# Optimization experiments

Hardware: AMD Instinct MI355X
Metric: run time of the kernel (lower is better)

The kernel has to match this reference:

```python
import jax, jax.numpy as jnp
import numpy as np

B, T, EMB, HS = 4, 4096, 1024, 64
BASE = 10000.0


def rope_angles(T, hs, base=BASE):
    # theta_i = base^(-2i/hs), freqs[t, i] = t * theta_i  -> (T, hs//2)
    inv = 1.0 / (base ** (2.0 * jnp.arange(hs // 2, dtype=jnp.float32) / hs))
    return jnp.arange(T, dtype=jnp.float32)[:, None] * inv[None, :]


def apply_rope(x, cos, sin):
    # x: (B, T, D); pairs are interleaved (even, odd) like torch.view_as_complex
    xr = x.reshape(*x.shape[:-1], -1, 2)
    xe, xo = xr[..., 0], xr[..., 1]
    re = xe * cos - xo * sin
    im = xe * sin + xo * cos
    return jnp.stack([re, im], axis=-1).reshape(x.shape)


def setup_inputs() -> dict:
    key = jax.random.key(0)
    kx, kq, kk, kv = jax.random.split(key, 4)
    s = 1.0 / np.sqrt(EMB)
    return {
        "x": jax.random.normal(kx, (B, T, EMB), jnp.float32),
        "Wq": jax.random.normal(kq, (HS, EMB), jnp.float32) * s,
        "Wk": jax.random.normal(kk, (HS, EMB), jnp.float32) * s,
        "Wv": jax.random.normal(kv, (HS, EMB), jnp.float32) * s,
    }


def reference(x, Wq, Wk, Wv):
    Tlen = x.shape[1]
    ang = rope_angles(Tlen, HS)          # (T, HS//2)
    cos, sin = jnp.cos(ang), jnp.sin(ang)
    q = x @ Wq.T                          # (B, T, HS)
    k = x @ Wk.T
    v = x @ Wv.T
    q = apply_rope(q, cos, sin)
    k = apply_rope(k, cos, sin)
    scores = jnp.einsum("bqd,bkd->bqk", q, k) * (HS ** -0.5)
    causal = jnp.tril(jnp.ones((Tlen, Tlen), dtype=bool))
    scores = jnp.where(causal[None], scores, -jnp.inf)
    w = jax.nn.softmax(scores, axis=-1)   # dropout in eval mode: identity
    return jnp.einsum("bqk,bkd->bqd", w, v)
```

## Files before the change

### kernel.cpp

```cpp
#include <hip/hip_runtime.h>

typedef __bf16 bf16x8 __attribute__((ext_vector_type(8)));
typedef __bf16 bf16x4 __attribute__((ext_vector_type(4)));
typedef float f32x4 __attribute__((ext_vector_type(4)));
typedef float f32x16 __attribute__((ext_vector_type(16)));
typedef unsigned int u32;

#define T_LEN 4096

__device__ __forceinline__ f32x4 mfma16(bf16x8 a, bf16x8 b, f32x4 c) {
    return __builtin_amdgcn_mfma_f32_16x16x32_bf16(a, b, c, 0, 0, 0);
}
__device__ __forceinline__ f32x16 mfma32(bf16x8 a, bf16x8 b, f32x16 c) {
    return __builtin_amdgcn_mfma_f32_32x32x16_bf16(a, b, c, 0, 0, 0);
}
__device__ __forceinline__ u32 packbf(float lo, float hi) {
    union { __bf16 e[2]; u32 w; } u;
    u.e[0] = (__bf16)lo; u.e[1] = (__bf16)hi;
    return u.w;
}
__device__ __forceinline__ f32x16 zero16() {
    f32x16 z;
    #pragma unroll
    for (int i = 0; i < 16; i++) z[i] = 0.f;
    return z;
}

__global__ __launch_bounds__(256) void convert_w_kernel(
    const float* __restrict__ Wq, const float* __restrict__ Wk,
    const float* __restrict__ Wv, __bf16* __restrict__ wb)
{
    int i = blockIdx.x * 256 + threadIdx.x;
    int m = i >> 14, off = (i & 16383) << 2;
    const float* s = (m == 0 ? Wq : (m == 1 ? Wk : Wv)) + off;
    float4 f = *(const float4*)s;
    bf16x4 h = { (__bf16)f.x, (__bf16)f.y, (__bf16)f.z, (__bf16)f.w };
    *(bf16x4*)(wb + (m << 16) + off) = h;
}

__global__ __launch_bounds__(512, 2) void proj_kernel(
    const float* __restrict__ x, const __bf16* __restrict__ wb,
    __bf16* __restrict__ qfb, __bf16* __restrict__ kfb, __bf16* __restrict__ vfb)
{
    __shared__ __bf16 smem[4608 + 27648];
    __bf16 (*xs)[32][72]  = (__bf16(*)[32][72])smem;
    __bf16 (*wl)[192][72] = (__bf16(*)[192][72])(smem + 4608);
    __bf16* stage = smem;

    const int tid  = threadIdx.x;
    const int wave = tid >> 6, lane = tid & 63;
    const int l15 = lane & 15, l4 = lane >> 4;
    const int wm = wave >> 2, wn = wave & 3;
    const size_t m0 = (size_t)blockIdx.x * 32;
    const int xrow = tid >> 4, xc4 = (tid & 15) * 4;
    const int wrow = tid >> 3, wcp = (tid & 7) * 8;

    f32x4 acc[3];
    #pragma unroll
    for (int bn = 0; bn < 3; bn++) acc[bn] = (f32x4){0.f, 0.f, 0.f, 0.f};

    const float* xsrc = x + (m0 + xrow) * 1024 + xc4;

    float4 rxA, rxB;
    bf16x8 rw[3];

    {
        float4 r0 = *(const float4*)(xsrc);
        bf16x4 hx = {(__bf16)r0.x, (__bf16)r0.y, (__bf16)r0.z, (__bf16)r0.w};
        *(bf16x4*)&xs[0][xrow][xc4] = hx;
        #pragma unroll
        for (int j = 0; j < 3; j++) {
            rw[j] = *(const bf16x8*)(wb + (size_t)(wrow + j * 64) * 1024 + wcp);
            *(bf16x8*)&wl[0][wrow + j * 64][wcp] = rw[j];
        }
        rxA = *(const float4*)(xsrc + 64);
    }
    __syncthreads();

    for (int t = 0; t < 16; t++) {
        const int cur = t & 1;
        if (t < 14)
            rxB = *(const float4*)(xsrc + (t + 2) * 64);
        if (t < 15) {
            const int k0 = (t + 1) * 64;
            #pragma unroll
            for (int j = 0; j < 3; j++)
                rw[j] = *(const bf16x8*)(wb + (size_t)(wrow + j * 64) * 1024 + k0 + wcp);
        }
        bf16x8 af[2], bfr[3][2];
        #pragma unroll
        for (int c = 0; c < 2; c++)
            af[c] = *(const bf16x8*)&xs[cur][wm * 16 + l15][c * 32 + l4 * 8];
        #pragma unroll
        for (int nf = 0; nf < 3; nf++)
            #pragma unroll
            for (int c = 0; c < 2; c++)
                bfr[nf][c] = *(const bf16x8*)&wl[cur][wn * 48 + nf * 16 + l15][c * 32 + l4 * 8];
        #pragma unroll
        for (int nf = 0; nf < 3; nf++)
            #pragma unroll
            for (int c = 0; c < 2; c++)
                acc[nf] = mfma16(af[c], bfr[nf][c], acc[nf]);
        if (t < 15) {
            bf16x4 hx = {(__bf16)rxA.x, (__bf16)rxA.y, (__bf16)rxA.z, (__bf16)rxA.w};
            *(bf16x4*)&xs[cur ^ 1][xrow][xc4] = hx;
            #pragma unroll
            for (int j = 0; j < 3; j++)
                *(bf16x8*)&wl[cur ^ 1][wrow + j * 64][wcp] = rw[j];
        }
        rxA = rxB;
        __syncthreads();
    }

    const int tq0 = (int)(m0 & 4095);
    #pragma unroll
    for (int nf = 0; nf < 3; nf++) {
        int n = wn * 48 + nf * 16 + l15;
        #pragma unroll
        for (int r = 0; r < 4; r++) {
            int row = wm * 16 + l4 * 4 + r;
            float val = acc[nf][r];
            float partner = __shfl_xor(val, 1);
            if (n < 128) {
                int i = (n & 63) >> 1;
                float ang = (float)(tq0 + row)
                          * __builtin_exp2f((float)i * (-13.287712379549449f / 32.f));
                float sn, cs;
                __sincosf(ang, &sn, &cs);
                float res = (n & 1) ? (partner * sn + val * cs)
                                    : (val * cs - partner * sn);
                if (n < 64) {
                    res *= 0.180336884f;
                    int d = n;
                    stage[(d >> 4) * 512 + (row + ((d >> 3) & 1) * 32) * 8 + (d & 7)]
                        = (__bf16)res;
                } else {
                    int d = n - 64;
                    int l31i = ((row >> 2) & 1) * 16 + ((row >> 4) & 1) * 8
                             + ((row >> 3) & 1) * 4 + (row & 3);
                    stage[2048 + (d >> 4) * 512
                          + (l31i + ((d >> 3) & 1) * 32) * 8 + (d & 7)] = (__bf16)res;
                }
            } else {
                int d = n - 128;
                int cc = ((d >> 5) << 1) | ((row & 31) >> 4);
                stage[4096 + cc * 512
                      + ((d & 31) + ((row >> 3) & 1) * 32) * 8 + (row & 7)]
                    = (__bf16)val;
            }
        }
    }
    __syncthreads();
    {
        const size_t bbase = (size_t)(m0 >> 12) * 262144;
        const size_t tbase = (size_t)((m0 & 4095) >> 5) * 2048;
        bf16x4 q4 = *(const bf16x4*)&stage[tid * 4];
        bf16x4 k4 = *(const bf16x4*)&stage[2048 + tid * 4];
        bf16x4 v4 = *(const bf16x4*)&stage[4096 + tid * 4];
        *(bf16x4*)(qfb + bbase + tbase + tid * 4) = q4;
        *(bf16x4*)(kfb + bbase + tbase + tid * 4) = k4;
        *(bf16x4*)(vfb + bbase + tbase + tid * 4) = v4;
    }
}

__global__ __launch_bounds__(1024) void flash_kernel(
    const __bf16* __restrict__ qfb, const __bf16* __restrict__ kfb,
    const __bf16* __restrict__ vfb, float* __restrict__ out)
{
    __shared__ float ods[16][32][36];
    __shared__ float mls[2][16][32];

    const int tid = threadIdx.x;
    const int wave = tid >> 6, lane = tid & 63;
    const int l31 = lane & 31, h = lane >> 5;
    const int xcd = blockIdx.x & 7;
    const int b = xcd >> 1;
    const int p = ((blockIdx.x >> 3) << 1) | (xcd & 1);

    const __bf16* qb_b = qfb + (size_t)b * 262144;
    const __bf16* kb_b = kfb + (size_t)b * 262144;
    const __bf16* vb_b = vfb + (size_t)b * 262144;

    #pragma unroll 1
    for (int half = 0; half < 2; half++) {
        const int jt = half ? p : 127 - p;
        const int q0 = jt * 32;
        const int qg = q0 + l31;

        const __bf16* qp = qb_b + (size_t)jt * 2048 + lane * 8;
        bf16x8 qf[4];
        #pragma unroll
        for (int dc = 0; dc < 4; dc++) qf[dc] = *(const bf16x8*)(qp + dc * 512);

        float m = 16.f, l = 0.f;
        f32x16 o0 = zero16(), o1 = zero16();
        const int nt = jt + 1;

        #pragma unroll 1
        for (int kt = wave; kt < nt; kt += 16) {
            const int kc0 = kt << 5;
            const __bf16* kr = kb_b + (size_t)kt * 2048 + lane * 8;
            bf16x8 kf0 = *(const bf16x8*)(kr);
            bf16x8 kf1 = *(const bf16x8*)(kr + 512);
            bf16x8 kf2 = *(const bf16x8*)(kr + 1024);
            bf16x8 kf3 = *(const bf16x8*)(kr + 1536);
            const __bf16* vr = vb_b + (size_t)kt * 2048 + lane * 8;
            bf16x8 vf00 = *(const bf16x8*)(vr);
            bf16x8 vf01 = *(const bf16x8*)(vr + 512);
            bf16x8 vf10 = *(const bf16x8*)(vr + 1024);
            bf16x8 vf11 = *(const bf16x8*)(vr + 1536);
            f32x16 s = zero16();
            __builtin_amdgcn_s_setprio(1);
            s = mfma32(kf0, qf[0], s);
            s = mfma32(kf1, qf[1], s);
            s = mfma32(kf2, qf[2], s);
            s = mfma32(kf3, qf[3], s);
            __builtin_amdgcn_s_setprio(0);
            if (kt == jt) {
                #pragma unroll
                for (int r = 0; r < 16; r++) {
                    int pioff = ((r >> 2) & 1) * 16 + 8 * h + (r >> 3) * 4 + (r & 3);
                    if (kc0 + pioff > qg) s[r] = -1e30f;
                }
            }
            float tm[8];
            #pragma unroll
            for (int i = 0; i < 8; i++) tm[i] = fmaxf(s[2 * i], s[2 * i + 1]);
            #pragma unroll
            for (int i = 0; i < 4; i++) tm[i] = fmaxf(tm[i], tm[i + 4]);
            float tmax = fmaxf(fmaxf(tm[0], tm[1]), fmaxf(tm[2], tm[3]));
            float ts[4] = {0.f, 0.f, 0.f, 0.f};
            #pragma unroll
            for (int r = 0; r < 16; r++) {
                float e = __builtin_exp2f(s[r] - m);
                s[r] = e;
                ts[r & 3] += e;
            }
            float lsum = (ts[0] + ts[1]) + (ts[2] + ts[3]);
            float lsum_p = __shfl_xor(lsum, 32);
            float tmax_p = __shfl_xor(tmax, 32);
            union { u32 w[4]; bf16x8 v; } pf[2];
            #pragma unroll
            for (int cg = 0; cg < 2; cg++) {
                pf[cg].w[0] = packbf(s[4 * cg + 0],  s[4 * cg + 1]);
                pf[cg].w[1] = packbf(s[4 * cg + 2],  s[4 * cg + 3]);
                pf[cg].w[2] = packbf(s[4 * cg + 8],  s[4 * cg + 9]);
                pf[cg].w[3] = packbf(s[4 * cg + 10], s[4 * cg + 11]);
            }
            __builtin_amdgcn_s_setprio(1);
            o0 = mfma32(vf00, pf[0].v, o0);
            o0 = mfma32(vf01, pf[1].v, o0);
            o1 = mfma32(vf10, pf[0].v, o1);
            o1 = mfma32(vf11, pf[1].v, o1);
            __builtin_amdgcn_s_setprio(0);
            l += lsum + lsum_p;
            float tmx = fmaxf(tmax, tmax_p);
            if (!__all(tmx <= m + 8.f)) {
                const float mnew = fmaxf(m, tmx);
                const float alpha = __builtin_exp2f(m - mnew);
                m = mnew;
                l *= alpha;
                #pragma unroll
                for (int r = 0; r < 16; r++) { o0[r] *= alpha; o1[r] *= alpha; }
            }
        }

        const int q = tid >> 5, dcm = tid & 31;
        #pragma unroll
        for (int c2 = 0; c2 < 4; c2++) {
            f32x4 w0 = {o0[4 * c2], o0[4 * c2 + 1], o0[4 * c2 + 2], o0[4 * c2 + 3]};
            *(f32x4*)&ods[wave][l31][8 * c2 + 4 * h] = w0;
        }
        if (h == 0) {
            mls[0][wave][l31] = (wave < nt) ? m : -1e30f;
            mls[1][wave][l31] = l;
        }
        __syncthreads();
        float M = -1e30f;
        #pragma unroll
        for (int s2 = 0; s2 < 16; s2++) M = fmaxf(M, mls[0][s2][q]);
        float w16[16], L = 0.f;
        #pragma unroll
        for (int s2 = 0; s2 < 16; s2++) {
            float ws = __builtin_exp2f(mls[0][s2][q] - M);
            w16[s2] = ws;
            L += ws * mls[1][s2][q];
        }
        const float invL = 1.f / L;
        float accA = 0.f;
        #pragma unroll
        for (int s2 = 0; s2 < 16; s2++) accA += w16[s2] * ods[s2][q][dcm];
        out[((size_t)b * T_LEN + q0 + q) * 64 + dcm] = accA * invL;
        __syncthreads();
        #pragma unroll
        for (int c2 = 0; c2 < 4; c2++) {
            f32x4 w1 = {o1[4 * c2], o1[4 * c2 + 1], o1[4 * c2 + 2], o1[4 * c2 + 3]};
            *(f32x4*)&ods[wave][l31][8 * c2 + 4 * h] = w1;
        }
        __syncthreads();
        float accB = 0.f;
        #pragma unroll
        for (int s2 = 0; s2 < 16; s2++) accB += w16[s2] * ods[s2][q][dcm];
        out[((size_t)b * T_LEN + q0 + q) * 64 + 32 + dcm] = accB * invL;
        __syncthreads();
    }
}

extern "C" void kernel_launch(void* const* d_in, const int* in_sizes, int n_in,
                              void* d_out, int out_size, void* d_ws, size_t ws_size,
                              hipStream_t stream)
{
    const float* x  = (const float*)d_in[0];
    const float* Wq = (const float*)d_in[1];
    const float* Wk = (const float*)d_in[2];
    const float* Wv = (const float*)d_in[3];
    float* out = (float*)d_out;

    __bf16* qfb = (__bf16*)d_ws;
    __bf16* kfb = qfb + 1048576;
    __bf16* vfb = kfb + 1048576;
    __bf16* wb  = vfb + 1048576;

    convert_w_kernel<<<192, 256, 0, stream>>>(Wq, Wk, Wv, wb);
    proj_kernel<<<512, 512, 0, stream>>>(x, wb, qfb, kfb, vfb);
    flash_kernel<<<256, 1024, 0, stream>>>(qfb, kfb, vfb, out);
}
```

Baseline: 54.13 us.

## Pre-swizzle weights into MFMA fragment order and load B-fragments straight from global

```diff
diff --git a/kernel.cpp b/kernel.cpp
--- a/kernel.cpp
+++ b/kernel.cpp
@@ -28,23 +28,28 @@
 
 __global__ __launch_bounds__(256) void convert_w_kernel(
     const float* __restrict__ Wq, const float* __restrict__ Wk,
-    const float* __restrict__ Wv, __bf16* __restrict__ wb)
+    const float* __restrict__ Wv, __bf16* __restrict__ wf)
 {
-    int i = blockIdx.x * 256 + threadIdx.x;
-    int m = i >> 14, off = (i & 16383) << 2;
-    const float* s = (m == 0 ? Wq : (m == 1 ? Wk : Wv)) + off;
-    float4 f = *(const float4*)s;
-    bf16x4 h = { (__bf16)f.x, (__bf16)f.y, (__bf16)f.z, (__bf16)f.w };
-    *(bf16x4*)(wb + (m << 16) + off) = h;
+    int e = (blockIdx.x * 256 + threadIdx.x) * 4;
+    int frag = e >> 9;
+    int wi = e & 511;
+    int l = wi >> 3, j = wi & 7;
+    int ft = frag / 12, fn = frag - ft * 12;
+    int n = fn * 16 + (l & 15);
+    int k = (ft >> 1) * 64 + (ft & 1) * 32 + ((l >> 4) & 3) * 8 + j;
+    const float* src = (n < 64 ? Wq : (n < 128 ? Wk : Wv))
+                     + (size_t)(n & 63) * 1024 + k;
+    float4 f = *(const float4*)src;
+    bf16x4 h = {(__bf16)f.x, (__bf16)f.y, (__bf16)f.z, (__bf16)f.w};
+    *(bf16x4*)(wf + e) = h;
 }
 
 __global__ __launch_bounds__(512, 2) void proj_kernel(
-    const float* __restrict__ x, const __bf16* __restrict__ wb,
+    const float* __restrict__ x, const __bf16* __restrict__ wf,
     __bf16* __restrict__ qfb, __bf16* __restrict__ kfb, __bf16* __restrict__ vfb)
 {
-    __shared__ __bf16 smem[4608 + 27648];
-    __bf16 (*xs)[32][72]  = (__bf16(*)[32][72])smem;
-    __bf16 (*wl)[192][72] = (__bf16(*)[192][72])(smem + 4608);
+    __shared__ __bf16 smem[6144];
+    __bf16 (*xs)[32][72] = (__bf16(*)[32][72])smem;
     __bf16* stage = smem;
 
     const int tid  = threadIdx.x;
@@ -53,27 +58,27 @@
     const int wm = wave >> 2, wn = wave & 3;
     const size_t m0 = (size_t)blockIdx.x * 32;
     const int xrow = tid >> 4, xc4 = (tid & 15) * 4;
-    const int wrow = tid >> 3, wcp = (tid & 7) * 8;
 
     f32x4 acc[3];
     #pragma unroll
     for (int bn = 0; bn < 3; bn++) acc[bn] = (f32x4){0.f, 0.f, 0.f, 0.f};
 
     const float* xsrc = x + (m0 + xrow) * 1024 + xc4;
+    const __bf16* wfw = wf + (size_t)(wn * 3) * 512 + lane * 8;
 
     float4 rxA, rxB;
-    bf16x8 rw[3];
+    bf16x8 wA[3][2], wB[3][2];
 
     {
         float4 r0 = *(const float4*)(xsrc);
         bf16x4 hx = {(__bf16)r0.x, (__bf16)r0.y, (__bf16)r0.z, (__bf16)r0.w};
         *(bf16x4*)&xs[0][xrow][xc4] = hx;
-        #pragma unroll
-        for (int j = 0; j < 3; j++) {
-            rw[j] = *(const bf16x8*)(wb + (size_t)(wrow + j * 64) * 1024 + wcp);
-            *(bf16x8*)&wl[0][wrow + j * 64][wcp] = rw[j];
-        }
         rxA = *(const float4*)(xsrc + 64);
+        #pragma unroll
+        for (int nf = 0; nf < 3; nf++)
+            #pragma unroll
+            for (int c = 0; c < 2; c++)
+                wA[nf][c] = *(const bf16x8*)(wfw + (size_t)(c * 12 + nf) * 512);
     }
     __syncthreads();
 
@@ -82,12 +87,14 @@
         if (t < 14)
             rxB = *(const float4*)(xsrc + (t + 2) * 64);
         if (t < 15) {
-            const int k0 = (t + 1) * 64;
-            #pragma unroll
-            for (int j = 0; j < 3; j++)
-                rw[j] = *(const bf16x8*)(wb + (size_t)(wrow + j * 64) * 1024 + k0 + wcp);
-        }
-        bf16x8 af[2], bfr[3][2];
+            const __bf16* wnx = wfw + (size_t)((t + 1) * 2) * 12 * 512;
+            #pragma unroll
+            for (int nf = 0; nf < 3; nf++)
+                #pragma unroll
+                for (int c = 0; c < 2; c++)
+                    wB[nf][c] = *(const bf16x8*)(wnx + (size_t)(c * 12 + nf) * 512);
+        }
+        bf16x8 af[2];
         #pragma unroll
         for (int c = 0; c < 2; c++)
             af[c] = *(const bf16x8*)&xs[cur][wm * 16 + l15][c * 32 + l4 * 8];
@@ -95,19 +102,16 @@
         for (int nf = 0; nf < 3; nf++)
             #pragma unroll
             for (int c = 0; c < 2; c++)
-                bfr[nf][c] = *(const bf16x8*)&wl[cur][wn * 48 + nf * 16 + l15][c * 32 + l4 * 8];
-        #pragma unroll
-        for (int nf = 0; nf < 3; nf++)
-            #pragma unroll
-            for (int c = 0; c < 2; c++)
-                acc[nf] = mfma16(af[c], bfr[nf][c], acc[nf]);
+                acc[nf] = mfma16(af[c], wA[nf][c], acc[nf]);
         if (t < 15) {
             bf16x4 hx = {(__bf16)rxA.x, (__bf16)rxA.y, (__bf16)rxA.z, (__bf16)rxA.w};
             *(bf16x4*)&xs[cur ^ 1][xrow][xc4] = hx;
-            #pragma unroll
-            for (int j = 0; j < 3; j++)
-                *(bf16x8*)&wl[cur ^ 1][wrow + j * 64][wcp] = rw[j];
-        }
+        }
+        #pragma unroll
+        for (int nf = 0; nf < 3; nf++)
+            #pragma unroll
+            for (int c = 0; c < 2; c++)
+                wA[nf][c] = wB[nf][c];
         rxA = rxB;
         __syncthreads();
     }
@@ -319,9 +323,9 @@
     __bf16* qfb = (__bf16*)d_ws;
     __bf16* kfb = qfb + 1048576;
     __bf16* vfb = kfb + 1048576;
-    __bf16* wb  = vfb + 1048576;
-
-    convert_w_kernel<<<192, 256, 0, stream>>>(Wq, Wk, Wv, wb);
-    proj_kernel<<<512, 512, 0, stream>>>(x, wb, qfb, kfb, vfb);
+    __bf16* wf  = vfb + 1048576;
+
+    convert_w_kernel<<<192, 256, 0, stream>>>(Wq, Wk, Wv, wf);
+    proj_kernel<<<512, 512, 0, stream>>>(x, wf, qfb, kfb, vfb);
     flash_kernel<<<256, 1024, 0, stream>>>(qfb, kfb, vfb, out);
 }
```

Measured after the change: 55.74 us. 1.03x slower.
